# Kernel optimization log

Measured on AMD Instinct MI355X. Metric: run time of the kernel, lower is better.

The kernel has to match this reference:

```python
import jax, jax.numpy as jnp
import numpy as np


def _dsepconv(inp, vert, horiz, offx, offy, mask):
    # inp: [B,C,H,W]; vert/horiz: [B,F,H,W]; offx/offy/mask: [B,F*F,H,W]
    B, C, H, W = inp.shape
    F = vert.shape[1]
    FF = F * F
    dt = inp.dtype
    k = jnp.arange(FF)
    ki = (k // F).astype(dt)   # vertical tap index i
    kj = (k % F).astype(dt)    # horizontal tap index j
    half = jnp.asarray((F - 1) / 2.0, dt)
    ys = jnp.arange(H, dtype=dt)
    xs = jnp.arange(W, dtype=dt)
    # per-pixel deformable sample positions, [B,FF,H,W]
    py = offy + ys[None, None, :, None] + (ki - half)[None, :, None, None]
    px = offx + xs[None, None, None, :] + (kj - half)[None, :, None, None]
    py = jnp.clip(py, 0.0, H - 1)
    px = jnp.clip(px, 0.0, W - 1)
    y0f = jnp.floor(py)
    x0f = jnp.floor(px)
    wy = py - y0f   # bilinear fractional weights
    wx = px - x0f
    y0 = y0f.astype(jnp.int32)
    x0 = x0f.astype(jnp.int32)
    y1 = jnp.minimum(y0 + 1, H - 1)
    x1 = jnp.minimum(x0 + 1, W - 1)

    inp_flat = inp.reshape(B, C, H * W)

    def gather(yi, xi):
        # flat spatial gather per batch element -> [B,C,FF,H,W]
        idx = (yi * W + xi).reshape(B, FF * H * W)
        g = jax.vmap(lambda im, ix: im[:, ix])(inp_flat, idx)
        return g.reshape(B, C, FF, H, W)

    g00 = gather(y0, x0)
    g01 = gather(y0, x1)
    g10 = gather(y1, x0)
    g11 = gather(y1, x1)
    wy_ = wy[:, None]  # [B,1,FF,H,W]
    wx_ = wx[:, None]
    samp = (g00 * (1 - wy_) * (1 - wx_)
            + g01 * (1 - wy_) * wx_
            + g10 * wy_ * (1 - wx_)
            + g11 * wy_ * wx_)  # [B,C,FF,H,W]
    # separable mask-weighted tap weights: vert[i]*horiz[j]*mask[k]
    wtap = vert[:, k // F] * horiz[:, k % F] * mask  # [B,FF,H,W]
    return jnp.einsum('bkhw,bckhw->bchw', wtap, samp)


def setup_inputs() -> dict:
    key = jax.random.key(0)
    ks = jax.random.split(key, 6)
    B, C, H, W, F = 4, 3, 384, 384, 5
    return {
        'tensorInput': jax.random.normal(ks[0], (B, C, H, W), jnp.float32),
        'tensorVertical': jax.random.uniform(ks[1], (B, F, H, W), jnp.float32),
        'tensorHorizontal': jax.random.uniform(ks[2], (B, F, H, W), jnp.float32),
        'tensorOffsetX': jax.random.normal(ks[3], (B, F * F, H, W), jnp.float32),
        'tensorOffsetY': jax.random.normal(ks[4], (B, F * F, H, W), jnp.float32),
        'tensorMask': jax.random.uniform(ks[5], (B, F * F, H, W), jnp.float32),
    }


def reference(tensorInput, tensorVertical, tensorHorizontal, tensorOffsetX, tensorOffsetY, tensorMask):
    return _dsepconv(tensorInput, tensorVertical, tensorHorizontal,
                     tensorOffsetX, tensorOffsetY, tensorMask)
```

## Files before the change

kernel.cpp:

```cpp
#include <hip/hip_runtime.h>
#include <hip/hip_fp16.h>

#define BB 4
#define CC 3
#define HH 384
#define WW 384
#define FF 5
#define KK 25
#define HW (HH*WW)
#define WP 192
#define TOT (BB*HH*WP)

#define TX 64
#define TY 8

typedef float fx2 __attribute__((ext_vector_type(2)));

__device__ __forceinline__ fx2 nt_load2(const float* p) {
    return __builtin_nontemporal_load((const fx2*)p);
}

__device__ __forceinline__ uint2 pack_px(float c0, float c1, float c2) {
    __half2 h01 = __floats2half2_rn(c0, c1);
    uint2 r;
    r.x = *(const unsigned int*)&h01;
    r.y = (unsigned int)__half_as_ushort(__float2half_rn(c2));
    return r;
}

__global__ __launch_bounds__(256) void pack_kernel(
    const float* __restrict__ inp, uint4* __restrict__ tab)
{
    int t = blockIdx.x * blockDim.x + threadIdx.x;
    if (t >= TOT) return;
    int j = t % WP;
    int y = (t / WP) % HH;
    int b = t / (WP * HH);
    int p0 = 2 * j, p1 = 2 * j + 1, p2 = min(2 * j + 2, WW - 1);
    const float* b0 = inp + (((size_t)b * CC + 0) * HH + y) * WW;
    const float* b1 = inp + (((size_t)b * CC + 1) * HH + y) * WW;
    const float* b2 = inp + (((size_t)b * CC + 2) * HH + y) * WW;
    uint2 q0 = pack_px(b0[p0], b1[p0], b2[p0]);
    uint2 q1 = pack_px(b0[p1], b1[p1], b2[p1]);
    uint2 q2 = pack_px(b0[p2], b1[p2], b2[p2]);
    tab[t]       = make_uint4(q0.x, q0.y, q1.x, q1.y);
    tab[TOT + t] = make_uint4(q1.x, q1.y, q2.x, q2.y);
}

__device__ __forceinline__ void unpack_pair(uint4 r,
    float& lo0, float& lo1, float& lo2, float& hi0, float& hi1, float& hi2)
{
    float2 lo01 = __half22float2(*(const __half2*)&r.x);
    float2 hi01 = __half22float2(*(const __half2*)&r.z);
    lo0 = lo01.x; lo1 = lo01.y;
    hi0 = hi01.x; hi1 = hi01.y;
    lo2 = __half2float(*(const __half*)&r.y);
    hi2 = __half2float(*(const __half*)&r.w);
}

__global__ __launch_bounds__(256) void dsepconv_kernel(
    const uint4* __restrict__ tab,
    const float* __restrict__ vert,
    const float* __restrict__ horiz,
    const float* __restrict__ offx,
    const float* __restrict__ offy,
    const float* __restrict__ mask,
    float* __restrict__ out)
{
    int tx = threadIdx.x & 31;
    int ty = threadIdx.x >> 5;
    int xb = blockIdx.x * TX + tx * 2;
    int y  = blockIdx.y * TY + ty;
    int b  = blockIdx.z;
    int planeoff = y * WW + xb;

    fx2 v2[FF], h2[FF];
#pragma unroll
    for (int f = 0; f < FF; ++f) {
        v2[f] = nt_load2(vert  + (b * FF + f) * HW + planeoff);
        h2[f] = nt_load2(horiz + (b * FF + f) * HW + planeoff);
    }

    const uint4* tb = tab + (size_t)b * (HH * WP);

    float acc[2][3] = {{0.f,0.f,0.f},{0.f,0.f,0.f}};
    const float fy = (float)y;

    for (int ki = 0; ki < FF; ++ki) {
        float dy = fy + (float)(ki - 2);
        const float* ox_p = offx + (size_t)(b * KK + ki * FF) * HW + planeoff;
        const float* oy_p = offy + (size_t)(b * KK + ki * FF) * HW + planeoff;
        const float* m_p  = mask + (size_t)(b * KK + ki * FF) * HW + planeoff;
#pragma unroll
        for (int kj = 0; kj < FF; ++kj) {
            fx2 ox2 = nt_load2(ox_p + kj * HW);
            fx2 oy2 = nt_load2(oy_p + kj * HW);
            fx2 m2  = nt_load2(m_p  + kj * HW);
#pragma unroll
            for (int p = 0; p < 2; ++p) {
                float wt = v2[ki][p] * h2[kj][p] * m2[p];
                float py = oy2[p] + dy;
                float px = ox2[p] + (float)(xb + p + kj - 2);
                py = fminf(fmaxf(py, 0.f), (float)(HH - 1));
                px = fminf(fmaxf(px, 0.f), (float)(WW - 1));
                float y0f = floorf(py);
                float x0f = floorf(px);
                float wy = py - y0f;
                float wx = px - x0f;
                int y0 = (int)y0f;
                int x0 = (int)x0f;
                int y1 = min(y0 + 1, HH - 1);

                int j    = x0 >> 1;
                const uint4* tbs = tb + ((x0 & 1) ? TOT : 0);
                uint4 r0 = tbs[y0 * WP + j];
                uint4 r1 = tbs[y1 * WP + j];

                float a00,a01,a02,b00,b01,b02;
                float a10,a11,a12,b10,b11,b12;
                unpack_pair(r0, a00,a01,a02, b00,b01,b02);
                unpack_pair(r1, a10,a11,a12, b10,b11,b12);

                float w00 = (1.f - wy) * (1.f - wx);
                float w01 = (1.f - wy) * wx;
                float w10 = wy * (1.f - wx);
                float w11 = wy * wx;

                acc[p][0] += wt * (a00*w00 + b00*w01 + a10*w10 + b10*w11);
                acc[p][1] += wt * (a01*w00 + b01*w01 + a11*w10 + b11*w11);
                acc[p][2] += wt * (a02*w00 + b02*w01 + a12*w10 + b12*w11);
            }
        }
    }

#pragma unroll
    for (int c = 0; c < CC; ++c) {
        fx2 o; o.x = acc[0][c]; o.y = acc[1][c];
        *(fx2*)(out + ((size_t)b * CC + c) * HW + planeoff) = o;
    }
}

extern "C" void kernel_launch(void* const* d_in, const int* in_sizes, int n_in,
                              void* d_out, int out_size, void* d_ws, size_t ws_size,
                              hipStream_t stream) {
    const float* inp   = (const float*)d_in[0];
    const float* vert  = (const float*)d_in[1];
    const float* horiz = (const float*)d_in[2];
    const float* offx  = (const float*)d_in[3];
    const float* offy  = (const float*)d_in[4];
    const float* mask  = (const float*)d_in[5];
    float* out = (float*)d_out;
    uint4* tab = (uint4*)d_ws;

    {
        pack_kernel<<<(TOT + 255) / 256, 256, 0, stream>>>(inp, tab);
    }
    {
        dim3 grid(WW / TX, HH / TY, BB);
        dsepconv_kernel<<<grid, 256, 0, stream>>>(
            tab, vert, horiz, offx, offy, mask, out);
    }
}
```

Baseline: 219.8 us.

## Stage packed input tile with halo in LDS for bilinear gathers

Replaces the duplicated paired-pixel global table with a simple per-pixel packed fp16 table. Each block loads an input tile plus a halo into shared memory, and bilinear taps read from LDS, falling back to global memory when a sample lands outside the halo. This aims to cut global gather traffic and shrink the pack step. In exchange each tap now does four LDS reads instead of two 16-byte global loads, adds a branch, costs LDS capacity per block and adds a barrier.

```diff
diff --git a/kernel.cpp b/kernel.cpp
--- a/kernel.cpp
+++ b/kernel.cpp
@@ -8,11 +8,13 @@
 #define FF 5
 #define KK 25
 #define HW (HH*WW)
-#define WP 192
-#define TOT (BB*HH*WP)
 
 #define TX 64
 #define TY 8
+#define MX 12
+#define MY 10
+#define SX (TX+2*MX)
+#define SY (TY+2*MY)
 
 typedef float fx2 __attribute__((ext_vector_type(2)));
 
@@ -28,38 +30,25 @@
     return r;
 }
 
+__device__ __forceinline__ void unpack_px(uint2 q, float& c0, float& c1, float& c2) {
+    float2 f01 = __half22float2(*(const __half2*)&q.x);
+    c0 = f01.x; c1 = f01.y;
+    c2 = __half2float(*(const __half*)&q.y);
+}
+
 __global__ __launch_bounds__(256) void pack_kernel(
-    const float* __restrict__ inp, uint4* __restrict__ tab)
+    const float* __restrict__ inp, uint2* __restrict__ tab)
 {
     int t = blockIdx.x * blockDim.x + threadIdx.x;
-    if (t >= TOT) return;
-    int j = t % WP;
-    int y = (t / WP) % HH;
-    int b = t / (WP * HH);
-    int p0 = 2 * j, p1 = 2 * j + 1, p2 = min(2 * j + 2, WW - 1);
-    const float* b0 = inp + (((size_t)b * CC + 0) * HH + y) * WW;
-    const float* b1 = inp + (((size_t)b * CC + 1) * HH + y) * WW;
-    const float* b2 = inp + (((size_t)b * CC + 2) * HH + y) * WW;
-    uint2 q0 = pack_px(b0[p0], b1[p0], b2[p0]);
-    uint2 q1 = pack_px(b0[p1], b1[p1], b2[p1]);
-    uint2 q2 = pack_px(b0[p2], b1[p2], b2[p2]);
-    tab[t]       = make_uint4(q0.x, q0.y, q1.x, q1.y);
-    tab[TOT + t] = make_uint4(q1.x, q1.y, q2.x, q2.y);
+    if (t >= BB * HW) return;
+    int b = t / HW;
+    int i = t - b * HW;
+    const float* base = inp + (size_t)b * CC * HW + i;
+    tab[t] = pack_px(base[0], base[HW], base[2 * HW]);
 }
 
-__device__ __forceinline__ void unpack_pair(uint4 r,
-    float& lo0, float& lo1, float& lo2, float& hi0, float& hi1, float& hi2)
-{
-    float2 lo01 = __half22float2(*(const __half2*)&r.x);
-    float2 hi01 = __half22float2(*(const __half2*)&r.z);
-    lo0 = lo01.x; lo1 = lo01.y;
-    hi0 = hi01.x; hi1 = hi01.y;
-    lo2 = __half2float(*(const __half*)&r.y);
-    hi2 = __half2float(*(const __half*)&r.w);
-}
-
-__global__ __launch_bounds__(256) void dsepconv_kernel(
-    const uint4* __restrict__ tab,
+__global__ __launch_bounds__(256, 4) void dsepconv_kernel(
+    const uint2* __restrict__ tab,
     const float* __restrict__ vert,
     const float* __restrict__ horiz,
     const float* __restrict__ offx,
@@ -67,11 +56,31 @@
     const float* __restrict__ mask,
     float* __restrict__ out)
 {
+    __shared__ uint2 sm[SY][SX];
+
+    int b  = blockIdx.z;
+    int X0 = blockIdx.x * TX;
+    int Y0 = blockIdx.y * TY;
+    int XS0 = X0 - MX;
+    int YS0 = Y0 - MY;
+
+    const uint2* tb = tab + (size_t)b * HW;
+
+    for (int c = threadIdx.x; c < SY * (SX / 2); c += 256) {
+        int sy  = c / (SX / 2);
+        int sxp = c - sy * (SX / 2);
+        int gy  = min(max(YS0 + sy, 0), HH - 1);
+        int gx0 = min(max(XS0 + 2 * sxp,     0), WW - 1);
+        int gx1 = min(max(XS0 + 2 * sxp + 1, 0), WW - 1);
+        sm[sy][2 * sxp]     = tb[gy * WW + gx0];
+        sm[sy][2 * sxp + 1] = tb[gy * WW + gx1];
+    }
+    __syncthreads();
+
     int tx = threadIdx.x & 31;
     int ty = threadIdx.x >> 5;
-    int xb = blockIdx.x * TX + tx * 2;
-    int y  = blockIdx.y * TY + ty;
-    int b  = blockIdx.z;
+    int xb = X0 + tx * 2;
+    int y  = Y0 + ty;
     int planeoff = y * WW + xb;
 
     fx2 v2[FF], h2[FF];
@@ -80,8 +89,6 @@
         v2[f] = nt_load2(vert  + (b * FF + f) * HW + planeoff);
         h2[f] = nt_load2(horiz + (b * FF + f) * HW + planeoff);
     }
-
-    const uint4* tb = tab + (size_t)b * (HH * WP);
 
     float acc[2][3] = {{0.f,0.f,0.f},{0.f,0.f,0.f}};
     const float fy = (float)y;
@@ -110,25 +117,38 @@
                 int y0 = (int)y0f;
                 int x0 = (int)x0f;
                 int y1 = min(y0 + 1, HH - 1);
+                int x1 = min(x0 + 1, WW - 1);
 
-                int j    = x0 >> 1;
-                const uint4* tbs = tb + ((x0 & 1) ? TOT : 0);
-                uint4 r0 = tbs[y0 * WP + j];
-                uint4 r1 = tbs[y1 * WP + j];
+                int sy0 = y0 - YS0, sy1 = y1 - YS0;
+                int sx0 = x0 - XS0, sx1 = x1 - XS0;
 
-                float a00,a01,a02,b00,b01,b02;
-                float a10,a11,a12,b10,b11,b12;
-                unpack_pair(r0, a00,a01,a02, b00,b01,b02);
-                unpack_pair(r1, a10,a11,a12, b10,b11,b12);
+                uint2 q00, q01, q10, q11;
+                if (sy0 >= 0 && sy1 < SY && sx0 >= 0 && sx1 < SX) {
+                    q00 = sm[sy0][sx0];
+                    q01 = sm[sy0][sx1];
+                    q10 = sm[sy1][sx0];
+                    q11 = sm[sy1][sx1];
+                } else {
+                    q00 = tb[y0 * WW + x0];
+                    q01 = tb[y0 * WW + x1];
+                    q10 = tb[y1 * WW + x0];
+                    q11 = tb[y1 * WW + x1];
+                }
+
+                float a0,a1,a2, b0,b1,b2, c0,c1,c2, d0,d1,d2;
+                unpack_px(q00, a0,a1,a2);
+                unpack_px(q01, b0,b1,b2);
+                unpack_px(q10, c0,c1,c2);
+                unpack_px(q11, d0,d1,d2);
 
                 float w00 = (1.f - wy) * (1.f - wx);
                 float w01 = (1.f - wy) * wx;
                 float w10 = wy * (1.f - wx);
                 float w11 = wy * wx;
 
-                acc[p][0] += wt * (a00*w00 + b00*w01 + a10*w10 + b10*w11);
-                acc[p][1] += wt * (a01*w00 + b01*w01 + a11*w10 + b11*w11);
-                acc[p][2] += wt * (a02*w00 + b02*w01 + a12*w10 + b12*w11);
+                acc[p][0] += wt * (a0*w00 + b0*w01 + c0*w10 + d0*w11);
+                acc[p][1] += wt * (a1*w00 + b1*w01 + c1*w10 + d1*w11);
+                acc[p][2] += wt * (a2*w00 + b2*w01 + c2*w10 + d2*w11);
             }
         }
     }
@@ -150,10 +170,11 @@
     const float* offy  = (const float*)d_in[4];
     const float* mask  = (const float*)d_in[5];
     float* out = (float*)d_out;
-    uint4* tab = (uint4*)d_ws;
+    uint2* tab = (uint2*)d_ws;
 
     {
-        pack_kernel<<<(TOT + 255) / 256, 256, 0, stream>>>(inp, tab);
+        int total = BB * HW;
+        pack_kernel<<<(total + 255) / 256, 256, 0, stream>>>(inp, tab);
     }
     {
         dim3 grid(WW / TX, HH / TY, BB);
```

Measured after the change: 345.3 us. +57.1%, slower.
